# Kernel tuning notes

Hardware: AMD Instinct MI355X
Metric: run time of the kernel (lower is better)

The kernel has to match this reference:

```python
import jax, jax.numpy as jnp
import numpy as np

HEADS = 12
HEAD_DIM = 64  # dim // heads = 768 // 12


def setup_inputs() -> dict:
    key = jax.random.key(0)
    ks = jax.random.split(key, 9)
    dim = 768
    B, N = 8, 1024
    s = 1.0 / np.sqrt(dim)
    return {
        "x": jax.random.normal(ks[0], (B, N, dim), jnp.float32),
        "Wq": jax.random.normal(ks[1], (dim, dim), jnp.float32) * s,
        "bq": jax.random.normal(ks[2], (dim,), jnp.float32) * 0.02,
        "Wk": jax.random.normal(ks[3], (dim, dim), jnp.float32) * s,
        "bk": jax.random.normal(ks[4], (dim,), jnp.float32) * 0.02,
        "Wv": jax.random.normal(ks[5], (dim, dim), jnp.float32) * s,
        "bv": jax.random.normal(ks[6], (dim,), jnp.float32) * 0.02,
        "Wo": jax.random.normal(ks[7], (dim, dim), jnp.float32) * s,
        "bo": jax.random.normal(ks[8], (dim,), jnp.float32) * 0.02,
    }


def _split_heads(t):
    # [B, N, H*D] -> [B, H, N, D]
    B, N, _ = t.shape
    return t.reshape(B, N, HEADS, HEAD_DIM).transpose(0, 2, 1, 3)


def reference(x, Wq, bq, Wk, bk, Wv, bv, Wo, bo):
    q = _split_heads(x @ Wq + bq)  # [B, H, N, D]
    k = _split_heads(x @ Wk + bk)
    v = _split_heads(x @ Wv + bv)
    scale = 1.0 / jnp.sqrt(jnp.asarray(HEAD_DIM, x.dtype))
    scores = jnp.einsum("bhid,bhjd->bhij", q, k) * scale  # [B, H, N, N]
    attn = jax.nn.softmax(scores, axis=-1)
    weights = attn  # use_vis=True
    o = jnp.einsum("bhij,bhjd->bhid", attn, v)  # [B, H, N, D]
    B, H, N, D = o.shape
    o = o.transpose(0, 2, 1, 3).reshape(B, N, H * D)  # [B, N, dim]
    out = o @ Wo + bo  # dropout_rate=0 -> identity
    return (out, weights)
```

## Files before the change

kernel.cpp:

```cpp
#include <hip/hip_runtime.h>
#include <hip/hip_bf16.h>
#include <stdint.h>


#define DIM 768
#define NHEADS 12
#define HDIM 64
#define BATCH 8
#define SEQ 1024
#define TOKENS (BATCH * SEQ)
#define NQKV (3 * DIM)

typedef __bf16 bf16x8 __attribute__((ext_vector_type(8)));
typedef float f32x4 __attribute__((ext_vector_type(4)));

__device__ __forceinline__ unsigned int f2bf(float f) {
  unsigned int x = __float_as_uint(f);
  return (x + 0x7fffu + ((x >> 16) & 1u)) >> 16;
}


__global__ __launch_bounds__(256) void conv_x_kernel(const float* __restrict__ x,
                                                     unsigned short* __restrict__ xb) {
  int i = blockIdx.x * 256 + threadIdx.x;
  float4 v = *((const float4*)x + i);
  uint2 o;
  o.x = f2bf(v.x) | (f2bf(v.y) << 16);
  o.y = f2bf(v.z) | (f2bf(v.w) << 16);
  *((uint2*)xb + i) = o;
}

__global__ __launch_bounds__(256) void transpose_w_kernel(const float* __restrict__ Wq,
                                                          const float* __restrict__ Wk,
                                                          const float* __restrict__ Wv,
                                                          const float* __restrict__ Wo,
                                                          unsigned short* __restrict__ WT) {
  __shared__ float tile[32][33];
  const float* W = (blockIdx.z == 0) ? Wq : (blockIdx.z == 1) ? Wk : (blockIdx.z == 2) ? Wv : Wo;
  int tx = threadIdx.x & 31, ty = threadIdx.x >> 5;
  int k0 = blockIdx.y * 32, n0 = blockIdx.x * 32;
#pragma unroll
  for (int r = ty; r < 32; r += 8) tile[r][tx] = W[(size_t)(k0 + r) * DIM + n0 + tx];
  __syncthreads();
  unsigned short* dst = WT + (size_t)blockIdx.z * DIM * DIM;
#pragma unroll
  for (int r = ty; r < 32; r += 8)
    dst[(size_t)(n0 + r) * DIM + k0 + tx] = (unsigned short)f2bf(tile[tx][r]);
}

__global__ __launch_bounds__(256) void pack_bias_kernel(const float* __restrict__ bq,
                                                        const float* __restrict__ bk,
                                                        const float* __restrict__ bv,
                                                        float* __restrict__ bqkv) {
  int i = blockIdx.x * 256 + threadIdx.x;
  if (i < NQKV) bqkv[i] = (i < DIM) ? bq[i] : (i < 2 * DIM) ? bk[i - DIM] : bv[i - 2 * DIM];
}


template <int MODE, typename TA>
__global__ __launch_bounds__(256) void gemm_bt_kernel(
    const TA* __restrict__ A, const unsigned short* __restrict__ B,
    const float* __restrict__ bias, float* __restrict__ outF,
    unsigned short* __restrict__ outA, unsigned short* __restrict__ outB,
    unsigned short* __restrict__ outC, int M, int N, int K, int lda, int ldb,
    long long strideA, long long strideB, float scale) {
  __shared__ alignas(16) unsigned short As[128 * 40];
  __shared__ alignas(16) unsigned short Bs[128 * 40];

  const int z = blockIdx.z;
  A += (long long)z * strideA;
  B += (long long)z * strideB;

  const int t = threadIdx.x;
  const int lane = t & 63;
  const int w = t >> 6;
  const int wm = w >> 1, wn = w & 1;
  const int quad = lane >> 4, l15 = lane & 15;
  const int bm = blockIdx.y, bn = blockIdx.x;

  const f32x4 zero4 = {0.f, 0.f, 0.f, 0.f};
  f32x4 acc[4][4];
#pragma unroll
  for (int i = 0; i < 4; i++)
#pragma unroll
    for (int j = 0; j < 4; j++) acc[i][j] = zero4;

  for (int bk = 0; bk < K; bk += 32) {
#pragma unroll
    for (int c = 0; c < 2; c++) {
      int chunk = t + c * 256;
      int row = chunk >> 2, seg = chunk & 3;
      long long g = (long long)(bm * 128 + row) * lda + bk + seg * 8;
      uint4 v;
      if constexpr (sizeof(TA) == 2) {
        v = *(const uint4*)((const unsigned short*)A + g);
      } else {
        const float* Af = (const float*)A + g;
        float4 f0 = *(const float4*)Af;
        float4 f1 = *(const float4*)(Af + 4);
        v.x = f2bf(f0.x) | (f2bf(f0.y) << 16);
        v.y = f2bf(f0.z) | (f2bf(f0.w) << 16);
        v.z = f2bf(f1.x) | (f2bf(f1.y) << 16);
        v.w = f2bf(f1.z) | (f2bf(f1.w) << 16);
      }
      *(uint4*)(&As[row * 40 + seg * 8]) = v;
    }
#pragma unroll
    for (int c = 0; c < 2; c++) {
      int chunk = t + c * 256;
      int row = chunk >> 2, seg = chunk & 3;
      int nrow = bn * 128 + row;
      uint4 v = make_uint4(0u, 0u, 0u, 0u);
      if (nrow < N) v = *(const uint4*)(B + (long long)nrow * ldb + bk + seg * 8);
      *(uint4*)(&Bs[row * 40 + seg * 8]) = v;
    }
    __syncthreads();

    bf16x8 a[4], b[4];
#pragma unroll
    for (int i = 0; i < 4; i++)
      a[i] = *(const bf16x8*)(&As[(wm * 64 + i * 16 + l15) * 40 + quad * 8]);
#pragma unroll
    for (int j = 0; j < 4; j++)
      b[j] = *(const bf16x8*)(&Bs[(wn * 64 + j * 16 + l15) * 40 + quad * 8]);
#pragma unroll
    for (int i = 0; i < 4; i++)
#pragma unroll
      for (int j = 0; j < 4; j++)
        acc[i][j] = __builtin_amdgcn_mfma_f32_16x16x32_bf16(a[i], b[j], acc[i][j], 0, 0, 0);
    __syncthreads();
  }

#pragma unroll
  for (int i = 0; i < 4; i++) {
#pragma unroll
    for (int j = 0; j < 4; j++) {
#pragma unroll
      for (int r = 0; r < 4; r++) {
        int row = bm * 128 + wm * 64 + i * 16 + quad * 4 + r;
        int col = bn * 128 + wn * 64 + j * 16 + l15;
        float v = acc[i][j][r];
        if constexpr (MODE == 0) {
          v += bias[col];
          int b_ = row >> 10, nseq = row & 1023;
          int wsel = col / DIM, nn = col - wsel * DIM;
          int h = nn >> 6, d = nn & 63;
          long long bh = (long long)b_ * NHEADS + h;
          if (wsel == 0)
            outA[(bh * SEQ + nseq) * HDIM + d] = (unsigned short)f2bf(v * 0.125f);
          else if (wsel == 1)
            outB[(bh * SEQ + nseq) * HDIM + d] = (unsigned short)f2bf(v);
          else
            outC[(bh * HDIM + d) * SEQ + nseq] = (unsigned short)f2bf(v);
        } else {
          outF[(long long)row * DIM + col] = v + bias[col];
        }
      }
    }
  }
  (void)scale;
  (void)outF;
}


__global__ __launch_bounds__(256, 2) void fused_attn_kernel(
    const unsigned short* __restrict__ qm, const unsigned short* __restrict__ km,
    const unsigned short* __restrict__ vm, float* __restrict__ probs,
    unsigned short* __restrict__ om) {
  __shared__ alignas(16) unsigned short Ks[128][72];
  __shared__ alignas(16) unsigned short Vs[64][136];
  __shared__ alignas(16) unsigned short Ps[128][136];

  const int z = blockIdx.y, mblk = blockIdx.x;
  const int bb = z / NHEADS, hh = z - bb * NHEADS;
  const unsigned short* qb = qm + (size_t)z * SEQ * HDIM;
  const unsigned short* kb = km + (size_t)z * SEQ * HDIM;
  const unsigned short* vb = vm + (size_t)z * HDIM * SEQ;
  float* pz = probs + (size_t)z * SEQ * SEQ;

  const int t = threadIdx.x;
  const int w = t >> 6;
  const int quad = (t & 63) >> 4, l15 = t & 15;
  const int rw = w * 32;

  bf16x8 aq[2][2];
#pragma unroll
  for (int i = 0; i < 2; i++)
#pragma unroll
    for (int kk = 0; kk < 2; kk++)
      aq[i][kk] = *(const bf16x8*)(qb + (size_t)(mblk * 128 + rw + i * 16 + l15) * HDIM +
                                   kk * 32 + quad * 8);

  float m[2][4], s[2][4];
#pragma unroll
  for (int i = 0; i < 2; i++)
#pragma unroll
    for (int r = 0; r < 4; r++) {
      m[i][r] = -1e30f;
      s[i][r] = 0.f;
    }

  const f32x4 zero4 = {0.f, 0.f, 0.f, 0.f};

  for (int jt = 0; jt < 8; jt++) {
#pragma unroll
    for (int c = 0; c < 4; c++) {
      int chunk = t + c * 256;
      int row = chunk >> 3, seg = chunk & 7;
      *(uint4*)(&Ks[row][seg * 8]) =
          *(const uint4*)(kb + (size_t)(jt * 128 + row) * HDIM + seg * 8);
    }
    __syncthreads();
    f32x4 acc[2][8];
#pragma unroll
    for (int i = 0; i < 2; i++)
#pragma unroll
      for (int j = 0; j < 8; j++) acc[i][j] = zero4;
#pragma unroll
    for (int j = 0; j < 8; j++) {
      bf16x8 b0 = *(const bf16x8*)(&Ks[j * 16 + l15][quad * 8]);
      bf16x8 b1 = *(const bf16x8*)(&Ks[j * 16 + l15][32 + quad * 8]);
#pragma unroll
      for (int i = 0; i < 2; i++) {
        acc[i][j] = __builtin_amdgcn_mfma_f32_16x16x32_bf16(aq[i][0], b0, acc[i][j], 0, 0, 0);
        acc[i][j] = __builtin_amdgcn_mfma_f32_16x16x32_bf16(aq[i][1], b1, acc[i][j], 0, 0, 0);
      }
    }
#pragma unroll
    for (int i = 0; i < 2; i++)
#pragma unroll
      for (int r = 0; r < 4; r++) {
        float tm = acc[i][0][r];
#pragma unroll
        for (int j = 1; j < 8; j++) tm = fmaxf(tm, acc[i][j][r]);
#pragma unroll
        for (int mk = 1; mk < 16; mk <<= 1) tm = fmaxf(tm, __shfl_xor(tm, mk, 64));
        float mn = fmaxf(m[i][r], tm);
        float se = 0.f;
#pragma unroll
        for (int j = 0; j < 8; j++) se += __expf(acc[i][j][r] - mn);
#pragma unroll
        for (int mk = 1; mk < 16; mk <<= 1) se += __shfl_xor(se, mk, 64);
        s[i][r] = s[i][r] * __expf(m[i][r] - mn) + se;
        m[i][r] = mn;
      }
    __syncthreads();
  }

  float is_[2][4];
#pragma unroll
  for (int i = 0; i < 2; i++)
#pragma unroll
    for (int r = 0; r < 4; r++) is_[i][r] = 1.0f / s[i][r];

  f32x4 oacc[2][4];
#pragma unroll
  for (int i = 0; i < 2; i++)
#pragma unroll
    for (int dj = 0; dj < 4; dj++) oacc[i][dj] = zero4;

  for (int jt = 0; jt < 8; jt++) {
#pragma unroll
    for (int c = 0; c < 4; c++) {
      int chunk = t + c * 256;
      int row = chunk >> 3, seg = chunk & 7;
      *(uint4*)(&Ks[row][seg * 8]) =
          *(const uint4*)(kb + (size_t)(jt * 128 + row) * HDIM + seg * 8);
    }
#pragma unroll
    for (int c = 0; c < 4; c++) {
      int chunk = t + c * 256;
      int row = chunk >> 4, seg = chunk & 15;
      *(uint4*)(&Vs[row][seg * 8]) =
          *(const uint4*)(vb + (size_t)row * SEQ + jt * 128 + seg * 8);
    }
    __syncthreads();
    f32x4 acc[2][8];
#pragma unroll
    for (int i = 0; i < 2; i++)
#pragma unroll
      for (int j = 0; j < 8; j++) acc[i][j] = zero4;
#pragma unroll
    for (int j = 0; j < 8; j++) {
      bf16x8 b0 = *(const bf16x8*)(&Ks[j * 16 + l15][quad * 8]);
      bf16x8 b1 = *(const bf16x8*)(&Ks[j * 16 + l15][32 + quad * 8]);
#pragma unroll
      for (int i = 0; i < 2; i++) {
        acc[i][j] = __builtin_amdgcn_mfma_f32_16x16x32_bf16(aq[i][0], b0, acc[i][j], 0, 0, 0);
        acc[i][j] = __builtin_amdgcn_mfma_f32_16x16x32_bf16(aq[i][1], b1, acc[i][j], 0, 0, 0);
      }
    }
#pragma unroll
    for (int i = 0; i < 2; i++)
#pragma unroll
      for (int j = 0; j < 8; j++) {
        int colg = jt * 128 + j * 16 + l15;
#pragma unroll
        for (int r = 0; r < 4; r++) {
          float p = __expf(acc[i][j][r] - m[i][r]) * is_[i][r];
          int rloc = rw + i * 16 + quad * 4 + r;
          pz[(size_t)(mblk * 128 + rloc) * SEQ + colg] = p;
          Ps[rloc][j * 16 + l15] = (unsigned short)f2bf(p);
        }
      }
#pragma unroll
    for (int kk = 0; kk < 4; kk++) {
      bf16x8 ap0 = *(const bf16x8*)(&Ps[rw + l15][kk * 32 + quad * 8]);
      bf16x8 ap1 = *(const bf16x8*)(&Ps[rw + 16 + l15][kk * 32 + quad * 8]);
#pragma unroll
      for (int dj = 0; dj < 4; dj++) {
        bf16x8 bv = *(const bf16x8*)(&Vs[dj * 16 + l15][kk * 32 + quad * 8]);
        oacc[0][dj] = __builtin_amdgcn_mfma_f32_16x16x32_bf16(ap0, bv, oacc[0][dj], 0, 0, 0);
        oacc[1][dj] = __builtin_amdgcn_mfma_f32_16x16x32_bf16(ap1, bv, oacc[1][dj], 0, 0, 0);
      }
    }
    __syncthreads();
  }

#pragma unroll
  for (int i = 0; i < 2; i++)
#pragma unroll
    for (int dj = 0; dj < 4; dj++)
#pragma unroll
      for (int r = 0; r < 4; r++) {
        int orow = mblk * 128 + rw + i * 16 + quad * 4 + r;
        om[((size_t)(bb * SEQ + orow)) * DIM + hh * HDIM + dj * 16 + l15] =
            (unsigned short)f2bf(oacc[i][dj][r]);
      }
}


extern "C" void kernel_launch(void* const* d_in, const int* in_sizes, int n_in,
                              void* d_out, int out_size, void* d_ws, size_t ws_size,
                              hipStream_t stream) {
  const float* x = (const float*)d_in[0];
  const float* Wq = (const float*)d_in[1];
  const float* bq = (const float*)d_in[2];
  const float* Wk = (const float*)d_in[3];
  const float* bk = (const float*)d_in[4];
  const float* Wv = (const float*)d_in[5];
  const float* bv = (const float*)d_in[6];
  const float* Wo = (const float*)d_in[7];
  const float* bo = (const float*)d_in[8];

  char* ws = (char*)d_ws;
  size_t off = 0;
  auto alloc = [&](size_t bytes) {
    void* p = ws + off;
    off = (off + bytes + 255) & ~(size_t)255;
    return p;
  };
  unsigned short* xb = (unsigned short*)alloc((size_t)TOKENS * DIM * 2);
  unsigned short* WT = (unsigned short*)alloc((size_t)4 * DIM * DIM * 2);
  float* bqkv = (float*)alloc((size_t)NQKV * 4);
  unsigned short* q = (unsigned short*)alloc((size_t)TOKENS * DIM * 2);
  unsigned short* kmat = (unsigned short*)alloc((size_t)TOKENS * DIM * 2);
  unsigned short* vT = (unsigned short*)alloc((size_t)TOKENS * DIM * 2);
  unsigned short* o = (unsigned short*)alloc((size_t)TOKENS * DIM * 2);
  (void)ws_size;

  float* outp = (float*)d_out;
  float* probs = outp + (size_t)TOKENS * DIM;

  conv_x_kernel<<<(TOKENS * DIM / 4) / 256, 256, 0, stream>>>(x, xb);
  transpose_w_kernel<<<dim3(24, 24, 4), 256, 0, stream>>>(Wq, Wk, Wv, Wo, WT);
  pack_bias_kernel<<<9, 256, 0, stream>>>(bq, bk, bv, bqkv);

  gemm_bt_kernel<0, unsigned short><<<dim3(18, 64, 1), 256, 0, stream>>>(
      xb, WT, bqkv, nullptr, q, kmat, vT, TOKENS, NQKV, DIM, DIM, DIM, 0, 0, 0.f);

  fused_attn_kernel<<<dim3(8, 96), 256, 0, stream>>>(q, kmat, vT, probs, o);

  gemm_bt_kernel<3, unsigned short><<<dim3(6, 64, 1), 256, 0, stream>>>(
      o, WT + (size_t)3 * DIM * DIM, bo, outp, nullptr, nullptr, nullptr, TOKENS, DIM, DIM,
      DIM, DIM, 0, 0, 0.f);
}
```

Baseline: 660.5 us.

## Use direct global-to-LDS loads with XOR swizzle; add V transpose kernel

Replaces register-staged global→LDS copies in the GEMM and attention kernels with global_load_lds 16-byte direct loads into unpadded, XOR-swizzled shared tiles, shrinking LDS and avoiding bank conflicts. The QKV GEMM now writes V in head-major layout, and a separate transpose kernel produces V^T, avoiding the strided scattered stores from the GEMM epilogue. The attention probability writes become nontemporal stores to keep the large probs stream out of cache. It adds an extra kernel launch and an extra pass over V.

```diff
diff --git a/kernel.cpp b/kernel.cpp
--- a/kernel.cpp
+++ b/kernel.cpp
@@ -17,6 +17,12 @@
 __device__ __forceinline__ unsigned int f2bf(float f) {
   unsigned int x = __float_as_uint(f);
   return (x + 0x7fffu + ((x >> 16) & 1u)) >> 16;
+}
+
+__device__ __forceinline__ void gload16(const void* g, void* l) {
+  __builtin_amdgcn_global_load_lds(
+      (const __attribute__((address_space(1))) void*)g,
+      (__attribute__((address_space(3))) void*)l, 16, 0, 0);
 }
 
 
@@ -56,20 +62,35 @@
   if (i < NQKV) bqkv[i] = (i < DIM) ? bq[i] : (i < 2 * DIM) ? bk[i - DIM] : bv[i - 2 * DIM];
 }
 
-
-template <int MODE, typename TA>
+__global__ __launch_bounds__(256) void transpose_v_kernel(const unsigned short* __restrict__ v,
+                                                          unsigned short* __restrict__ vT) {
+  __shared__ unsigned short td[64][66];
+  const int z = blockIdx.y;
+  const int n0 = blockIdx.x * 64;
+  const unsigned short* vb = v + (size_t)z * SEQ * HDIM;
+  unsigned short* ob = vT + (size_t)z * HDIM * SEQ;
+  const int t = threadIdx.x;
+  const int rr = t >> 2, cc = (t & 3) * 16;
+  *(uint4*)&td[rr][cc] = *(const uint4*)(vb + (size_t)(n0 + rr) * HDIM + cc);
+  *(uint4*)&td[rr][cc + 8] = *(const uint4*)(vb + (size_t)(n0 + rr) * HDIM + cc + 8);
+  __syncthreads();
+  const int d = t >> 2, ns = (t & 3) * 16;
+  union { uint4 q[2]; unsigned short u[16]; } tmp;
+#pragma unroll
+  for (int e = 0; e < 16; e++) tmp.u[e] = td[ns + e][d];
+  *(uint4*)(ob + (size_t)d * SEQ + n0 + ns) = tmp.q[0];
+  *(uint4*)(ob + (size_t)d * SEQ + n0 + ns + 8) = tmp.q[1];
+}
+
+
+template <int MODE>
 __global__ __launch_bounds__(256) void gemm_bt_kernel(
-    const TA* __restrict__ A, const unsigned short* __restrict__ B,
+    const unsigned short* __restrict__ A, const unsigned short* __restrict__ B,
     const float* __restrict__ bias, float* __restrict__ outF,
-    unsigned short* __restrict__ outA, unsigned short* __restrict__ outB,
-    unsigned short* __restrict__ outC, int M, int N, int K, int lda, int ldb,
-    long long strideA, long long strideB, float scale) {
-  __shared__ alignas(16) unsigned short As[128 * 40];
-  __shared__ alignas(16) unsigned short Bs[128 * 40];
-
-  const int z = blockIdx.z;
-  A += (long long)z * strideA;
-  B += (long long)z * strideB;
+    unsigned short* __restrict__ outQ, unsigned short* __restrict__ outK,
+    unsigned short* __restrict__ outV, int K, int lda, int ldb) {
+  __shared__ alignas(16) unsigned short As[128 * 32];
+  __shared__ alignas(16) unsigned short Bs[128 * 32];
 
   const int t = threadIdx.x;
   const int lane = t & 63;
@@ -78,6 +99,12 @@
   const int quad = lane >> 4, l15 = lane & 15;
   const int bm = blockIdx.y, bn = blockIdx.x;
 
+  const int srow = lane >> 2;
+  const int segl = lane & 3;
+
+  const unsigned short* Abase = A + (size_t)(bm * 128) * lda;
+  const unsigned short* Bbase = B + (size_t)(bn * 128) * ldb;
+
   const f32x4 zero4 = {0.f, 0.f, 0.f, 0.f};
   f32x4 acc[4][4];
 #pragma unroll
@@ -88,41 +115,25 @@
   for (int bk = 0; bk < K; bk += 32) {
 #pragma unroll
     for (int c = 0; c < 2; c++) {
-      int chunk = t + c * 256;
-      int row = chunk >> 2, seg = chunk & 3;
-      long long g = (long long)(bm * 128 + row) * lda + bk + seg * 8;
-      uint4 v;
-      if constexpr (sizeof(TA) == 2) {
-        v = *(const uint4*)((const unsigned short*)A + g);
-      } else {
-        const float* Af = (const float*)A + g;
-        float4 f0 = *(const float4*)Af;
-        float4 f1 = *(const float4*)(Af + 4);
-        v.x = f2bf(f0.x) | (f2bf(f0.y) << 16);
-        v.y = f2bf(f0.z) | (f2bf(f0.w) << 16);
-        v.z = f2bf(f1.x) | (f2bf(f1.y) << 16);
-        v.w = f2bf(f1.z) | (f2bf(f1.w) << 16);
-      }
-      *(uint4*)(&As[row * 40 + seg * 8]) = v;
-    }
-#pragma unroll
-    for (int c = 0; c < 2; c++) {
-      int chunk = t + c * 256;
-      int row = chunk >> 2, seg = chunk & 3;
-      int nrow = bn * 128 + row;
-      uint4 v = make_uint4(0u, 0u, 0u, 0u);
-      if (nrow < N) v = *(const uint4*)(B + (long long)nrow * ldb + bk + seg * 8);
-      *(uint4*)(&Bs[row * 40 + seg * 8]) = v;
+      int g = w * 2 + c;
+      int row = g * 16 + srow;
+      int segg = segl ^ ((row >> 1) & 3);
+      gload16(Abase + (size_t)row * lda + bk + segg * 8, &As[g * 512]);
+      gload16(Bbase + (size_t)row * ldb + bk + segg * 8, &Bs[g * 512]);
     }
     __syncthreads();
 
     bf16x8 a[4], b[4];
 #pragma unroll
-    for (int i = 0; i < 4; i++)
-      a[i] = *(const bf16x8*)(&As[(wm * 64 + i * 16 + l15) * 40 + quad * 8]);
-#pragma unroll
-    for (int j = 0; j < 4; j++)
-      b[j] = *(const bf16x8*)(&Bs[(wn * 64 + j * 16 + l15) * 40 + quad * 8]);
+    for (int i = 0; i < 4; i++) {
+      int r = wm * 64 + i * 16 + l15;
+      a[i] = *(const bf16x8*)(&As[r * 32 + ((quad ^ ((r >> 1) & 3)) * 8)]);
+    }
+#pragma unroll
+    for (int j = 0; j < 4; j++) {
+      int r = wn * 64 + j * 16 + l15;
+      b[j] = *(const bf16x8*)(&Bs[r * 32 + ((quad ^ ((r >> 1) & 3)) * 8)]);
+    }
 #pragma unroll
     for (int i = 0; i < 4; i++)
 #pragma unroll
@@ -139,27 +150,24 @@
       for (int r = 0; r < 4; r++) {
         int row = bm * 128 + wm * 64 + i * 16 + quad * 4 + r;
         int col = bn * 128 + wn * 64 + j * 16 + l15;
-        float v = acc[i][j][r];
+        float v = acc[i][j][r] + bias[col];
         if constexpr (MODE == 0) {
-          v += bias[col];
           int b_ = row >> 10, nseq = row & 1023;
           int wsel = col / DIM, nn = col - wsel * DIM;
           int h = nn >> 6, d = nn & 63;
-          long long bh = (long long)b_ * NHEADS + h;
+          size_t idx = ((size_t)(b_ * NHEADS + h) * SEQ + nseq) * HDIM + d;
           if (wsel == 0)
-            outA[(bh * SEQ + nseq) * HDIM + d] = (unsigned short)f2bf(v * 0.125f);
+            outQ[idx] = (unsigned short)f2bf(v * 0.125f);
           else if (wsel == 1)
-            outB[(bh * SEQ + nseq) * HDIM + d] = (unsigned short)f2bf(v);
+            outK[idx] = (unsigned short)f2bf(v);
           else
-            outC[(bh * HDIM + d) * SEQ + nseq] = (unsigned short)f2bf(v);
+            outV[idx] = (unsigned short)f2bf(v);
         } else {
-          outF[(long long)row * DIM + col] = v + bias[col];
+          outF[(size_t)row * DIM + col] = v;
         }
       }
     }
   }
-  (void)scale;
-  (void)outF;
 }
 
 
@@ -167,8 +175,8 @@
     const unsigned short* __restrict__ qm, const unsigned short* __restrict__ km,
     const unsigned short* __restrict__ vm, float* __restrict__ probs,
     unsigned short* __restrict__ om) {
-  __shared__ alignas(16) unsigned short Ks[128][72];
-  __shared__ alignas(16) unsigned short Vs[64][136];
+  __shared__ alignas(16) unsigned short Ks[128 * 64];
+  __shared__ alignas(16) unsigned short Vs[64 * 128];
   __shared__ alignas(16) unsigned short Ps[128][136];
 
   const int z = blockIdx.y, mblk = blockIdx.x;
@@ -179,8 +187,9 @@
   float* pz = probs + (size_t)z * SEQ * SEQ;
 
   const int t = threadIdx.x;
+  const int lane = t & 63;
   const int w = t >> 6;
-  const int quad = (t & 63) >> 4, l15 = t & 15;
+  const int quad = lane >> 4, l15 = lane & 15;
   const int rw = w * 32;
 
   bf16x8 aq[2][2];
@@ -205,10 +214,10 @@
   for (int jt = 0; jt < 8; jt++) {
 #pragma unroll
     for (int c = 0; c < 4; c++) {
-      int chunk = t + c * 256;
-      int row = chunk >> 3, seg = chunk & 7;
-      *(uint4*)(&Ks[row][seg * 8]) =
-          *(const uint4*)(kb + (size_t)(jt * 128 + row) * HDIM + seg * 8);
+      int g = w * 4 + c;
+      int row = g * 8 + (lane >> 3);
+      int segg = (lane & 7) ^ (row & 7);
+      gload16(kb + (size_t)(jt * 128 + row) * HDIM + segg * 8, &Ks[g * 512]);
     }
     __syncthreads();
     f32x4 acc[2][8];
@@ -218,8 +227,9 @@
       for (int j = 0; j < 8; j++) acc[i][j] = zero4;
 #pragma unroll
     for (int j = 0; j < 8; j++) {
-      bf16x8 b0 = *(const bf16x8*)(&Ks[j * 16 + l15][quad * 8]);
-      bf16x8 b1 = *(const bf16x8*)(&Ks[j * 16 + l15][32 + quad * 8]);
+      int kr = j * 16 + l15;
+      bf16x8 b0 = *(const bf16x8*)(&Ks[kr * 64 + ((quad ^ (kr & 7)) * 8)]);
+      bf16x8 b1 = *(const bf16x8*)(&Ks[kr * 64 + (((4 + quad) ^ (kr & 7)) * 8)]);
 #pragma unroll
       for (int i = 0; i < 2; i++) {
         acc[i][j] = __builtin_amdgcn_mfma_f32_16x16x32_bf16(aq[i][0], b0, acc[i][j], 0, 0, 0);
@@ -262,17 +272,17 @@
   for (int jt = 0; jt < 8; jt++) {
 #pragma unroll
     for (int c = 0; c < 4; c++) {
-      int chunk = t + c * 256;
-      int row = chunk >> 3, seg = chunk & 7;
-      *(uint4*)(&Ks[row][seg * 8]) =
-          *(const uint4*)(kb + (size_t)(jt * 128 + row) * HDIM + seg * 8);
+      int g = w * 4 + c;
+      int row = g * 8 + (lane >> 3);
+      int segg = (lane & 7) ^ (row & 7);
+      gload16(kb + (size_t)(jt * 128 + row) * HDIM + segg * 8, &Ks[g * 512]);
     }
 #pragma unroll
     for (int c = 0; c < 4; c++) {
-      int chunk = t + c * 256;
-      int row = chunk >> 4, seg = chunk & 15;
-      *(uint4*)(&Vs[row][seg * 8]) =
-          *(const uint4*)(vb + (size_t)row * SEQ + jt * 128 + seg * 8);
+      int g = w * 4 + c;
+      int row = g * 4 + (lane >> 4);
+      int segg = (lane & 15) ^ (row & 15);
+      gload16(vb + (size_t)row * SEQ + jt * 128 + segg * 8, &Vs[g * 512]);
     }
     __syncthreads();
     f32x4 acc[2][8];
@@ -282,8 +292,9 @@
       for (int j = 0; j < 8; j++) acc[i][j] = zero4;
 #pragma unroll
     for (int j = 0; j < 8; j++) {
-      bf16x8 b0 = *(const bf16x8*)(&Ks[j * 16 + l15][quad * 8]);
-      bf16x8 b1 = *(const bf16x8*)(&Ks[j * 16 + l15][32 + quad * 8]);
+      int kr = j * 16 + l15;
+      bf16x8 b0 = *(const bf16x8*)(&Ks[kr * 64 + ((quad ^ (kr & 7)) * 8)]);
+      bf16x8 b1 = *(const bf16x8*)(&Ks[kr * 64 + (((4 + quad) ^ (kr & 7)) * 8)]);
 #pragma unroll
       for (int i = 0; i < 2; i++) {
         acc[i][j] = __builtin_amdgcn_mfma_f32_16x16x32_bf16(aq[i][0], b0, acc[i][j], 0, 0, 0);
@@ -299,7 +310,7 @@
         for (int r = 0; r < 4; r++) {
           float p = __expf(acc[i][j][r] - m[i][r]) * is_[i][r];
           int rloc = rw + i * 16 + quad * 4 + r;
-          pz[(size_t)(mblk * 128 + rloc) * SEQ + colg] = p;
+          __builtin_nontemporal_store(p, &pz[(size_t)(mblk * 128 + rloc) * SEQ + colg]);
           Ps[rloc][j * 16 + l15] = (unsigned short)f2bf(p);
         }
       }
@@ -309,7 +320,8 @@
       bf16x8 ap1 = *(const bf16x8*)(&Ps[rw + 16 + l15][kk * 32 + quad * 8]);
 #pragma unroll
       for (int dj = 0; dj < 4; dj++) {
-        bf16x8 bv = *(const bf16x8*)(&Vs[dj * 16 + l15][kk * 32 + quad * 8]);
+        int vr = dj * 16 + l15;
+        bf16x8 bv = *(const bf16x8*)(&Vs[vr * 128 + (((kk * 4 + quad) ^ (vr & 15)) * 8)]);
         oacc[0][dj] = __builtin_amdgcn_mfma_f32_16x16x32_bf16(ap0, bv, oacc[0][dj], 0, 0, 0);
         oacc[1][dj] = __builtin_amdgcn_mfma_f32_16x16x32_bf16(ap1, bv, oacc[1][dj], 0, 0, 0);
       }
@@ -366,12 +378,13 @@
   transpose_w_kernel<<<dim3(24, 24, 4), 256, 0, stream>>>(Wq, Wk, Wv, Wo, WT);
   pack_bias_kernel<<<9, 256, 0, stream>>>(bq, bk, bv, bqkv);
 
-  gemm_bt_kernel<0, unsigned short><<<dim3(18, 64, 1), 256, 0, stream>>>(
-      xb, WT, bqkv, nullptr, q, kmat, vT, TOKENS, NQKV, DIM, DIM, DIM, 0, 0, 0.f);
+  gemm_bt_kernel<0><<<dim3(18, 64), 256, 0, stream>>>(xb, WT, bqkv, nullptr, q, kmat, o,
+                                                      DIM, DIM, DIM);
+
+  transpose_v_kernel<<<dim3(16, 96), 256, 0, stream>>>(o, vT);
 
   fused_attn_kernel<<<dim3(8, 96), 256, 0, stream>>>(q, kmat, vT, probs, o);
 
-  gemm_bt_kernel<3, unsigned short><<<dim3(6, 64, 1), 256, 0, stream>>>(
-      o, WT + (size_t)3 * DIM * DIM, bo, outp, nullptr, nullptr, nullptr, TOKENS, DIM, DIM,
-      DIM, DIM, 0, 0, 0.f);
-}
+  gemm_bt_kernel<1><<<dim3(6, 64), 256, 0, stream>>>(o, WT + (size_t)3 * DIM * DIM, bo, outp,
+                                                     nullptr, nullptr, nullptr, DIM, DIM, DIM);
+}
```

Result: faster. 624.6 us (-5.4%).
